# Optimization experiments

Measured on AMD Instinct MI355X. Metric: run time of the kernel, lower is better.

The kernel has to match this reference:

```python
import jax, jax.numpy as jnp
import numpy as np

N_NODES = 10000
N_EDGES = 160000
D = 42          # node_input_dim == node_hidden_dim
DE = 10         # edge_input_dim
DEH = 42        # edge_hidden_dim
N_STEPS = 6


def setup_inputs() -> dict:
    key = jax.random.key(0)
    ks = jax.random.split(key, 16)
    s = 0.1
    return {
        "n_feat": jax.random.normal(ks[0], (N_NODES, D), jnp.float32),
        "e_feat": jax.random.normal(ks[1], (N_EDGES, DE), jnp.float32),
        "src": jax.random.randint(ks[2], (N_EDGES,), 0, N_NODES),
        "dst": jax.random.randint(ks[3], (N_EDGES,), 0, N_NODES),
        # lin0: node_input_dim -> node_hidden_dim
        "lin0_w": s * jax.random.normal(ks[4], (D, D), jnp.float32),
        "lin0_b": s * jax.random.normal(ks[5], (D,), jnp.float32),
        # message_layer: hidden -> hidden
        "msg_w": s * jax.random.normal(ks[6], (D, D), jnp.float32),
        "msg_b": s * jax.random.normal(ks[7], (D,), jnp.float32),
        # edge_network: Linear(10,42) -> ReLU -> Linear(42, 42*42)
        "en_w1": s * jax.random.normal(ks[8], (DE, DEH), jnp.float32),
        "en_b1": s * jax.random.normal(ks[9], (DEH,), jnp.float32),
        "en_w2": s * jax.random.normal(ks[10], (DEH, D * D), jnp.float32),
        "en_b2": s * jax.random.normal(ks[11], (D * D,), jnp.float32),
        # NNConv bias (DGL NNConv has bias=True by default)
        "conv_b": s * jax.random.normal(ks[12], (D,), jnp.float32),
    }


def reference(n_feat, e_feat, src, dst,
              lin0_w, lin0_b, msg_w, msg_b,
              en_w1, en_b1, en_w2, en_b2, conv_b):
    N, d = n_feat.shape
    init = n_feat
    out = jax.nn.relu(n_feat @ lin0_w + lin0_b)                      # [N, d]
    # Per-edge weight matrices from edge features (e_feat is constant
    # across steps, so the edge MLP is hoisted out of the loop).
    w_edge = (jax.nn.relu(e_feat @ en_w1 + en_b1) @ en_w2 + en_b2)   # [E, d*d]
    w_edge = w_edge.reshape(-1, d, d)                                # [E, d_in, d_out]
    for _ in range(N_STEPS):
        # NNConv: gather src feats, per-edge matvec, scatter-sum to dst
        msgs = jnp.einsum('ei,eio->eo', out[src], w_edge)            # [E, d]
        agg = jax.ops.segment_sum(msgs, dst, num_segments=N)         # [N, d]
        # residual (in==out -> identity res_fc) + bias, then outer ReLU
        m = jax.nn.relu(agg + out + conv_b)
        out = jax.nn.relu(m @ msg_w + msg_b)
    return out + init
```

## Files before the change

### kernel.cpp

```cpp
#include <hip/hip_runtime.h>
#include <hip/hip_bf16.h>


#define N_NODES 10000
#define N_EDGES 160000
#define D 42
#define DE 10
#define XSTR 48
#define HSTR 48
#define KI 1806
#define NKSTEP 57
#define SSTR 1832

typedef __attribute__((ext_vector_type(8))) short short8;
typedef __attribute__((ext_vector_type(4))) float f32x4;

static __device__ __forceinline__ short bf16b(float x) {
    __hip_bfloat16 h = __float2bfloat16(x);
    return *reinterpret_cast<short*>(&h);
}

__global__ __launch_bounds__(256) void k_lin0(const float* __restrict__ nf,
        const float* __restrict__ w, const float* __restrict__ b,
        float* __restrict__ out) {
    int idx = blockIdx.x * 256 + threadIdx.x;
    if (idx >= N_NODES * XSTR) return;
    int n = idx / XSTR, j = idx % XSTR;
    float v = 0.f;
    if (j < D) {
        const float* row = nf + n * D;
        float acc = b[j];
        #pragma unroll
        for (int i = 0; i < D; ++i) acc = fmaf(row[i], w[i * D + j], acc);
        v = fmaxf(acc, 0.f);
    }
    out[idx] = v;
}

__global__ __launch_bounds__(256) void k_T2B(const float* __restrict__ w2,
        const float* __restrict__ b2, __hip_bfloat16* __restrict__ Bfr) {
    int idx = blockIdx.x * 256 + threadIdx.x;
    if (idx >= 3 * NKSTEP * 64 * 8) return;
    int j = idx & 7, lane = (idx >> 3) & 63;
    int ks = (idx >> 9) % NKSTEP, nt = idx / (NKSTEP * 512);
    int col = nt * 16 + (lane & 15);
    int k = ks * 32 + ((lane >> 4) * 8) + j;
    float v = 0.f;
    if (col < D && k < KI) {
        int kk = k / D, ii = k % D;
        v = (kk < D) ? w2[kk * (D * D) + ii * D + col] : b2[ii * D + col];
    }
    Bfr[idx] = __float2bfloat16(v);
}

__global__ __launch_bounds__(256) void k_hist(const int* __restrict__ dst,
        int* __restrict__ cnt) {
    int e = blockIdx.x * 256 + threadIdx.x;
    if (e < N_EDGES) atomicAdd(&cnt[dst[e]], 1);
}

__global__ __launch_bounds__(1024) void k_scan(const int* __restrict__ cnt,
        int* __restrict__ row_ptr, int* __restrict__ cursor) {
    __shared__ int buf[1024];
    __shared__ int s_run;
    const int t = threadIdx.x;
    if (t == 0) s_run = 0;
    __syncthreads();
    for (int base = 0; base < N_NODES; base += 1024) {
        int v = (base + t < N_NODES) ? cnt[base + t] : 0;
        buf[t] = v;
        __syncthreads();
        for (int off = 1; off < 1024; off <<= 1) {
            int add = (t >= off) ? buf[t - off] : 0;
            __syncthreads();
            buf[t] += add;
            __syncthreads();
        }
        int excl = buf[t] - v;
        if (base + t < N_NODES) {
            int val = s_run + excl;
            row_ptr[base + t] = val;
            cursor[base + t]  = val;
        }
        __syncthreads();
        if (t == 0) s_run += buf[1023];
        __syncthreads();
    }
    if (t == 0) { row_ptr[N_NODES] = s_run; cursor[N_NODES] = s_run; }
}

__global__ __launch_bounds__(256) void k_scatter(const int* __restrict__ dst,
        const int* __restrict__ src, int* __restrict__ cursor,
        int* __restrict__ srcp, int* __restrict__ pos) {
    int e = blockIdx.x * 256 + threadIdx.x;
    if (e < N_EDGES) {
        int p = atomicAdd(&cursor[dst[e]], 1);
        pos[e] = p;
        srcp[p] = src[e];
    }
}

__global__ __launch_bounds__(256) void k_h16(const float* __restrict__ ef,
        const float* __restrict__ w1, const float* __restrict__ b1,
        const int* __restrict__ pos, __hip_bfloat16* __restrict__ hp16) {
    int idx = blockIdx.x * 256 + threadIdx.x;
    if (idx >= N_EDGES * HSTR) return;
    int e = idx / HSTR, j = idx % HSTR;
    float v;
    if (j < D) {
        const float* row = ef + e * DE;
        float acc = b1[j];
        #pragma unroll
        for (int i = 0; i < DE; ++i) acc = fmaf(row[i], w1[i * D + j], acc);
        v = fmaxf(acc, 0.f);
    } else {
        v = (j == D) ? 1.0f : 0.0f;
    }
    hp16[(size_t)pos[e] * HSTR + j] = __float2bfloat16(v);
}

#define MFMA(A, B, C) C = __builtin_amdgcn_mfma_f32_16x16x32_bf16(A, B, C, 0, 0, 0)

__global__ __launch_bounds__(512) void k_step2(
        const __hip_bfloat16* __restrict__ hp16, const float* __restrict__ out_in,
        const int* __restrict__ srcp, const int* __restrict__ row_ptr,
        const __hip_bfloat16* __restrict__ Bfr,
        const float* __restrict__ nf, const float* __restrict__ msg_w,
        const float* __restrict__ msg_b, const float* __restrict__ conv_b,
        float* __restrict__ out_dst, int last) {
    __shared__ __align__(16) __hip_bfloat16 sS[16 * SSTR];
    __shared__ float sR[16 * 48];
    __shared__ float sM[16 * 48];
    const int t = threadIdx.x;
    const int wv = t >> 6;
    const int l = t & 63;
    const int g = l >> 4;
    const int cl = l & 15;
    const int n0 = blockIdx.x * 16;

    for (int i = t; i < 16 * 48; i += 512) sR[i] = 0.f;
    for (int i = t; i < 16 * 18; i += 512)
        sS[(i / 18) * SSTR + KI + (i % 18)] = __float2bfloat16(0.f);

    const short* hp_s = (const short*)hp16;
    for (int q = 0; q < 2; ++q) {
        const int nloc = wv * 2 + q;
        const int node = n0 + nloc;
        const int beg = row_ptr[node], end = row_ptr[node + 1];
        f32x4 c00 = {0.f,0.f,0.f,0.f}, c01 = c00, c02 = c00;
        f32x4 c10 = c00, c11 = c00, c12 = c00;
        f32x4 c20 = c00, c21 = c00, c22 = c00;
        for (int e0 = beg; e0 < end; e0 += 32) {
            short8 a0, a1, a2, b0, b1, b2;
            #pragma unroll
            for (int j = 0; j < 8; ++j) {
                int ppos = e0 + g * 8 + j;
                bool vld = ppos < end;
                int pc = vld ? ppos : end - 1;
                const short* hr = hp_s + (size_t)pc * HSTR + cl;
                short h0 = hr[0], h1 = hr[16], h2 = hr[32];
                a0[j] = vld ? h0 : (short)0;
                a1[j] = vld ? h1 : (short)0;
                a2[j] = vld ? h2 : (short)0;
                const float* xr = out_in + (size_t)srcp[pc] * XSTR + cl;
                b0[j] = bf16b(xr[0]);
                b1[j] = bf16b(xr[16]);
                b2[j] = bf16b(xr[32]);
            }
            MFMA(a0, b0, c00); MFMA(a0, b1, c01); MFMA(a0, b2, c02);
            MFMA(a1, b0, c10); MFMA(a1, b1, c11); MFMA(a1, b2, c12);
            MFMA(a2, b0, c20); MFMA(a2, b1, c21); MFMA(a2, b2, c22);
        }
        #define ST(ACC, MT, NT)                                              \
            _Pragma("unroll")                                                \
            for (int r = 0; r < 4; ++r) {                                    \
                int m = (MT) * 16 + g * 4 + r;                               \
                int col = (NT) * 16 + cl;                                    \
                if (m < 43 && col < D)                                       \
                    sS[nloc * SSTR + m * D + col] = __float2bfloat16(ACC[r]);\
            }
        ST(c00, 0, 0) ST(c01, 0, 1) ST(c02, 0, 2)
        ST(c10, 1, 0) ST(c11, 1, 1) ST(c12, 1, 2)
        ST(c20, 2, 0) ST(c21, 2, 1) ST(c22, 2, 2)
        #undef ST
    }
    __syncthreads();

    {
        const int ks0 = (wv == 0) ? 0 : (wv * 7 + 1);
        const int ks1 = wv * 7 + 8;
        f32x4 d0 = {0.f,0.f,0.f,0.f}, d1 = d0, d2 = d0;
        const short* sSrow = (const short*)sS + cl * SSTR + g * 8;
        const short* bb = (const short*)Bfr + (size_t)l * 8;
        for (int ks = ks0; ks < ks1; ++ks) {
            short8 a  = *(const short8*)(sSrow + ks * 32);
            short8 B0 = *(const short8*)(bb + (size_t)(0 * NKSTEP + ks) * 512);
            short8 B1 = *(const short8*)(bb + (size_t)(1 * NKSTEP + ks) * 512);
            short8 B2 = *(const short8*)(bb + (size_t)(2 * NKSTEP + ks) * 512);
            MFMA(a, B0, d0); MFMA(a, B1, d1); MFMA(a, B2, d2);
        }
        const int rl = g * 4;
        #pragma unroll
        for (int r = 0; r < 4; ++r) {
            atomicAdd(&sR[(rl + r) * 48 + cl],      d0[r]);
            atomicAdd(&sR[(rl + r) * 48 + 16 + cl], d1[r]);
            atomicAdd(&sR[(rl + r) * 48 + 32 + cl], d2[r]);
        }
    }
    __syncthreads();

    float* sW = (float*)sS;
    for (int i = t; i < D * D; i += 512) sW[i] = msg_w[i];
    for (int idx = t; idx < 16 * 48; idx += 512) {
        int nl_ = idx / 48, o = idx % 48;
        float mv = 0.f;
        if (o < D) {
            float v = sR[idx] + out_in[(size_t)(n0 + nl_) * XSTR + o] + conv_b[o];
            mv = fmaxf(v, 0.f);
        }
        sM[idx] = mv;
    }
    __syncthreads();

    for (int idx = t; idx < 16 * 48; idx += 512) {
        int nl_ = idx / 48, pcol = idx % 48;
        if (pcol < D) {
            float s = msg_b[pcol];
            #pragma unroll 6
            for (int o = 0; o < D; ++o)
                s = fmaf(sM[nl_ * 48 + o], sW[o * D + pcol], s);
            float v = fmaxf(s, 0.f);
            if (last) {
                v += nf[(size_t)(n0 + nl_) * D + pcol];
                out_dst[(size_t)(n0 + nl_) * D + pcol] = v;
            } else {
                out_dst[(size_t)(n0 + nl_) * XSTR + pcol] = v;
            }
        } else if (!last) {
            out_dst[(size_t)(n0 + nl_) * XSTR + pcol] = 0.f;
        }
    }
}

extern "C" void kernel_launch(void* const* d_in, const int* in_sizes, int n_in,
                              void* d_out, int out_size, void* d_ws, size_t ws_size,
                              hipStream_t stream) {
    const float* nf    = (const float*)d_in[0];
    const float* ef    = (const float*)d_in[1];
    const int*   src   = (const int*)d_in[2];
    const int*   dst   = (const int*)d_in[3];
    const float* lin0w = (const float*)d_in[4];
    const float* lin0b = (const float*)d_in[5];
    const float* msgw  = (const float*)d_in[6];
    const float* msgb  = (const float*)d_in[7];
    const float* enw1  = (const float*)d_in[8];
    const float* enb1  = (const float*)d_in[9];
    const float* enw2  = (const float*)d_in[10];
    const float* enb2  = (const float*)d_in[11];
    const float* convb = (const float*)d_in[12];

    char* p = (char*)d_ws;
    auto alloc = [&](size_t bytes) -> char* {
        char* r = p; p += (bytes + 255) & ~(size_t)255; return r;
    };
    float* outA = (float*)alloc((size_t)N_NODES * XSTR * 4);
    float* outB = (float*)alloc((size_t)N_NODES * XSTR * 4);
    __hip_bfloat16* hp16 = (__hip_bfloat16*)alloc((size_t)N_EDGES * HSTR * 2);
    __hip_bfloat16* Bfr  = (__hip_bfloat16*)alloc((size_t)3 * NKSTEP * 64 * 8 * 2);
    int* cnt    = (int*)alloc((N_NODES + 1) * 4);
    int* rowp   = (int*)alloc((N_NODES + 1) * 4);
    int* cur    = (int*)alloc((N_NODES + 1) * 4);
    int* srcp   = (int*)alloc((size_t)N_EDGES * 4);
    int* posb   = (int*)alloc((size_t)N_EDGES * 4);

    hipMemsetAsync(cnt, 0, (N_NODES + 1) * 4, stream);
    k_lin0<<<(N_NODES * XSTR + 255) / 256, 256, 0, stream>>>(nf, lin0w, lin0b, outA);
    k_T2B<<<(3 * NKSTEP * 64 * 8 + 255) / 256, 256, 0, stream>>>(enw2, enb2, Bfr);
    k_hist<<<(N_EDGES + 255) / 256, 256, 0, stream>>>(dst, cnt);
    k_scan<<<1, 1024, 0, stream>>>(cnt, rowp, cur);
    k_scatter<<<(N_EDGES + 255) / 256, 256, 0, stream>>>(dst, src, cur, srcp, posb);
    k_h16<<<(N_EDGES * HSTR + 255) / 256, 256, 0, stream>>>(ef, enw1, enb1, posb, hp16);

    const int tiles = N_NODES / 16;
    float* bufs[2] = {outA, outB};
    for (int s_i = 0; s_i < 6; ++s_i) {
        const float* cin = bufs[s_i % 2];
        float* cout = bufs[(s_i + 1) % 2];
        int last = (s_i == 5) ? 1 : 0;
        k_step2<<<tiles, 512, 0, stream>>>(hp16, cin, srcp, rowp, Bfr,
                                           nf, msgw, msgb, convb,
                                           last ? (float*)d_out : cout, last);
    }
}
```

Baseline: 350.0 us.

## Store node features in bf16, transpose edge hidden into 32-edge chunks, halve block

Node feature buffers become bf16 instead of fp32, which halves gather traffic and removes per-element conversion in the inner loop. The edge hidden activations are stored transposed in 32-edge chunks so each lane does vector short8 loads, with masking at node boundaries. Source indices are loaded as int4. Each wave now processes two nodes interleaved to expose more memory-level parallelism, and blocks shrink to 8 nodes and 256 threads, which raises occupancy but means each Bfr fragment is reused across only half as many nodes.

```diff
diff --git a/kernel.cpp b/kernel.cpp
--- a/kernel.cpp
+++ b/kernel.cpp
@@ -4,10 +4,10 @@
 
 #define N_NODES 10000
 #define N_EDGES 160000
+#define NCHK 5000
 #define D 42
 #define DE 10
 #define XSTR 48
-#define HSTR 48
 #define KI 1806
 #define NKSTEP 57
 #define SSTR 1832
@@ -15,14 +15,9 @@
 typedef __attribute__((ext_vector_type(8))) short short8;
 typedef __attribute__((ext_vector_type(4))) float f32x4;
 
-static __device__ __forceinline__ short bf16b(float x) {
-    __hip_bfloat16 h = __float2bfloat16(x);
-    return *reinterpret_cast<short*>(&h);
-}
-
 __global__ __launch_bounds__(256) void k_lin0(const float* __restrict__ nf,
         const float* __restrict__ w, const float* __restrict__ b,
-        float* __restrict__ out) {
+        __hip_bfloat16* __restrict__ out16) {
     int idx = blockIdx.x * 256 + threadIdx.x;
     if (idx >= N_NODES * XSTR) return;
     int n = idx / XSTR, j = idx % XSTR;
@@ -34,7 +29,7 @@
         for (int i = 0; i < D; ++i) acc = fmaf(row[i], w[i * D + j], acc);
         v = fmaxf(acc, 0.f);
     }
-    out[idx] = v;
+    out16[idx] = __float2bfloat16(v);
 }
 
 __global__ __launch_bounds__(256) void k_T2B(const float* __restrict__ w2,
@@ -91,106 +86,160 @@
 
 __global__ __launch_bounds__(256) void k_scatter(const int* __restrict__ dst,
         const int* __restrict__ src, int* __restrict__ cursor,
-        int* __restrict__ srcp, int* __restrict__ pos) {
+        int* __restrict__ srcp, int* __restrict__ eperm) {
     int e = blockIdx.x * 256 + threadIdx.x;
     if (e < N_EDGES) {
         int p = atomicAdd(&cursor[dst[e]], 1);
-        pos[e] = p;
         srcp[p] = src[e];
-    }
-}
-
-__global__ __launch_bounds__(256) void k_h16(const float* __restrict__ ef,
+        eperm[p] = e;
+    }
+}
+
+__global__ __launch_bounds__(256) void k_hT(const float* __restrict__ ef,
         const float* __restrict__ w1, const float* __restrict__ b1,
-        const int* __restrict__ pos, __hip_bfloat16* __restrict__ hp16) {
-    int idx = blockIdx.x * 256 + threadIdx.x;
-    if (idx >= N_EDGES * HSTR) return;
-    int e = idx / HSTR, j = idx % HSTR;
-    float v;
-    if (j < D) {
-        const float* row = ef + e * DE;
-        float acc = b1[j];
-        #pragma unroll
-        for (int i = 0; i < DE; ++i) acc = fmaf(row[i], w1[i * D + j], acc);
-        v = fmaxf(acc, 0.f);
-    } else {
-        v = (j == D) ? 1.0f : 0.0f;
-    }
-    hp16[(size_t)pos[e] * HSTR + j] = __float2bfloat16(v);
+        const int* __restrict__ eperm, __hip_bfloat16* __restrict__ hpT) {
+    const int c = blockIdx.x;
+    const int t = threadIdx.x;
+    for (int j = t; j < 48 * 32; j += 256) {
+        int k = j >> 5, ep = j & 31;
+        int e = eperm[c * 32 + ep];
+        float v;
+        if (k < D) {
+            const float* row = ef + (size_t)e * DE;
+            float acc = b1[k];
+            #pragma unroll
+            for (int i = 0; i < DE; ++i) acc = fmaf(row[i], w1[i * D + k], acc);
+            v = fmaxf(acc, 0.f);
+        } else {
+            v = (k == D) ? 1.0f : 0.f;
+        }
+        hpT[(size_t)c * 1536 + j] = __float2bfloat16(v);
+    }
 }
 
 #define MFMA(A, B, C) C = __builtin_amdgcn_mfma_f32_16x16x32_bf16(A, B, C, 0, 0, 0)
 
-__global__ __launch_bounds__(512) void k_step2(
-        const __hip_bfloat16* __restrict__ hp16, const float* __restrict__ out_in,
+__global__ __launch_bounds__(256) void k_step3(
+        const __hip_bfloat16* __restrict__ hpT,
+        const __hip_bfloat16* __restrict__ out_in,
         const int* __restrict__ srcp, const int* __restrict__ row_ptr,
         const __hip_bfloat16* __restrict__ Bfr,
         const float* __restrict__ nf, const float* __restrict__ msg_w,
         const float* __restrict__ msg_b, const float* __restrict__ conv_b,
-        float* __restrict__ out_dst, int last) {
-    __shared__ __align__(16) __hip_bfloat16 sS[16 * SSTR];
-    __shared__ float sR[16 * 48];
-    __shared__ float sM[16 * 48];
+        __hip_bfloat16* __restrict__ out16_dst, float* __restrict__ fout,
+        int last) {
+    __shared__ __align__(16) __hip_bfloat16 sS[8 * SSTR];
+    __shared__ float sR[8 * 48];
+    __shared__ float sM[8 * 48];
     const int t = threadIdx.x;
     const int wv = t >> 6;
     const int l = t & 63;
     const int g = l >> 4;
+    const int g8 = g * 8;
     const int cl = l & 15;
-    const int n0 = blockIdx.x * 16;
-
-    for (int i = t; i < 16 * 48; i += 512) sR[i] = 0.f;
-    for (int i = t; i < 16 * 18; i += 512)
+    const int n0 = blockIdx.x * 8;
+    const short* hpTs = (const short*)hpT;
+    const short* xs = (const short*)out_in;
+
+    for (int i = t; i < 8 * 48; i += 256) sR[i] = 0.f;
+    for (int i = t; i < 8 * 18; i += 256)
         sS[(i / 18) * SSTR + KI + (i % 18)] = __float2bfloat16(0.f);
 
-    const short* hp_s = (const short*)hp16;
-    for (int q = 0; q < 2; ++q) {
-        const int nloc = wv * 2 + q;
-        const int node = n0 + nloc;
-        const int beg = row_ptr[node], end = row_ptr[node + 1];
-        f32x4 c00 = {0.f,0.f,0.f,0.f}, c01 = c00, c02 = c00;
-        f32x4 c10 = c00, c11 = c00, c12 = c00;
-        f32x4 c20 = c00, c21 = c00, c22 = c00;
-        for (int e0 = beg; e0 < end; e0 += 32) {
-            short8 a0, a1, a2, b0, b1, b2;
+    const int nodeA = n0 + wv * 2, nodeB = nodeA + 1;
+    const int begA = row_ptr[nodeA], endA = row_ptr[nodeA + 1];
+    const int begB = endA, endB = row_ptr[nodeB + 1];
+    const int c0A = begA >> 5, ncA = (endA > begA) ? ((endA - 1) >> 5) - c0A + 1 : 0;
+    const int c0B = begB >> 5, ncB = (endB > begB) ? ((endB - 1) >> 5) - c0B + 1 : 0;
+    const int ncmax = max(ncA, ncB);
+
+    f32x4 cA[9], cB[9];
+    #pragma unroll
+    for (int i = 0; i < 9; ++i) { cA[i] = {0.f,0.f,0.f,0.f}; cB[i] = cA[i]; }
+
+    for (int ci = 0; ci < ncmax; ++ci) {
+        short8 aA0, aA1, aA2, bA0, bA1, bA2;
+        short8 aB0, aB1, aB2, bB0, bB1, bB2;
+        bool doA = ci < ncA, doB = ci < ncB;
+        if (doA) {
+            const int c = c0A + ci, c32 = c << 5;
+            const short* hb = hpTs + (size_t)c * 1536 + cl * 32 + g8;
+            aA0 = *(const short8*)(hb);
+            aA1 = *(const short8*)(hb + 16 * 32);
+            aA2 = *(const short8*)(hb + 32 * 32);
+            int4 s0 = *(const int4*)(srcp + c32 + g8);
+            int4 s1 = *(const int4*)(srcp + c32 + g8 + 4);
+            const int se[8] = {s0.x, s0.y, s0.z, s0.w, s1.x, s1.y, s1.z, s1.w};
             #pragma unroll
             for (int j = 0; j < 8; ++j) {
-                int ppos = e0 + g * 8 + j;
-                bool vld = ppos < end;
-                int pc = vld ? ppos : end - 1;
-                const short* hr = hp_s + (size_t)pc * HSTR + cl;
-                short h0 = hr[0], h1 = hr[16], h2 = hr[32];
-                a0[j] = vld ? h0 : (short)0;
-                a1[j] = vld ? h1 : (short)0;
-                a2[j] = vld ? h2 : (short)0;
-                const float* xr = out_in + (size_t)srcp[pc] * XSTR + cl;
-                b0[j] = bf16b(xr[0]);
-                b1[j] = bf16b(xr[16]);
-                b2[j] = bf16b(xr[32]);
-            }
-            MFMA(a0, b0, c00); MFMA(a0, b1, c01); MFMA(a0, b2, c02);
-            MFMA(a1, b0, c10); MFMA(a1, b1, c11); MFMA(a1, b2, c12);
-            MFMA(a2, b0, c20); MFMA(a2, b1, c21); MFMA(a2, b2, c22);
-        }
-        #define ST(ACC, MT, NT)                                              \
-            _Pragma("unroll")                                                \
-            for (int r = 0; r < 4; ++r) {                                    \
-                int m = (MT) * 16 + g * 4 + r;                               \
-                int col = (NT) * 16 + cl;                                    \
-                if (m < 43 && col < D)                                       \
-                    sS[nloc * SSTR + m * D + col] = __float2bfloat16(ACC[r]);\
-            }
-        ST(c00, 0, 0) ST(c01, 0, 1) ST(c02, 0, 2)
-        ST(c10, 1, 0) ST(c11, 1, 1) ST(c12, 1, 2)
-        ST(c20, 2, 0) ST(c21, 2, 1) ST(c22, 2, 2)
-        #undef ST
-    }
+                const short* xr = xs + (size_t)se[j] * XSTR + cl;
+                bA0[j] = xr[0]; bA1[j] = xr[16]; bA2[j] = xr[32];
+            }
+            if (c32 < begA || c32 + 32 > endA) {
+                #pragma unroll
+                for (int j = 0; j < 8; ++j) {
+                    int ep = c32 + g8 + j;
+                    if (ep < begA || ep >= endA) { aA0[j] = 0; aA1[j] = 0; aA2[j] = 0; }
+                }
+            }
+        }
+        if (doB) {
+            const int c = c0B + ci, c32 = c << 5;
+            const short* hb = hpTs + (size_t)c * 1536 + cl * 32 + g8;
+            aB0 = *(const short8*)(hb);
+            aB1 = *(const short8*)(hb + 16 * 32);
+            aB2 = *(const short8*)(hb + 32 * 32);
+            int4 s0 = *(const int4*)(srcp + c32 + g8);
+            int4 s1 = *(const int4*)(srcp + c32 + g8 + 4);
+            const int se[8] = {s0.x, s0.y, s0.z, s0.w, s1.x, s1.y, s1.z, s1.w};
+            #pragma unroll
+            for (int j = 0; j < 8; ++j) {
+                const short* xr = xs + (size_t)se[j] * XSTR + cl;
+                bB0[j] = xr[0]; bB1[j] = xr[16]; bB2[j] = xr[32];
+            }
+            if (c32 < begB || c32 + 32 > endB) {
+                #pragma unroll
+                for (int j = 0; j < 8; ++j) {
+                    int ep = c32 + g8 + j;
+                    if (ep < begB || ep >= endB) { aB0[j] = 0; aB1[j] = 0; aB2[j] = 0; }
+                }
+            }
+        }
+        if (doA) {
+            MFMA(aA0, bA0, cA[0]); MFMA(aA0, bA1, cA[1]); MFMA(aA0, bA2, cA[2]);
+            MFMA(aA1, bA0, cA[3]); MFMA(aA1, bA1, cA[4]); MFMA(aA1, bA2, cA[5]);
+            MFMA(aA2, bA0, cA[6]); MFMA(aA2, bA1, cA[7]); MFMA(aA2, bA2, cA[8]);
+        }
+        if (doB) {
+            MFMA(aB0, bB0, cB[0]); MFMA(aB0, bB1, cB[1]); MFMA(aB0, bB2, cB[2]);
+            MFMA(aB1, bB0, cB[3]); MFMA(aB1, bB1, cB[4]); MFMA(aB1, bB2, cB[5]);
+            MFMA(aB2, bB0, cB[6]); MFMA(aB2, bB1, cB[7]); MFMA(aB2, bB2, cB[8]);
+        }
+    }
+    #define ST(CC, NLOC, MT, NT)                                             \
+        _Pragma("unroll")                                                    \
+        for (int r = 0; r < 4; ++r) {                                        \
+            int m = (MT) * 16 + g * 4 + r;                                   \
+            int col = (NT) * 16 + cl;                                        \
+            if (m < 43 && col < D)                                           \
+                sS[(NLOC) * SSTR + m * D + col] = __float2bfloat16(CC[r]);   \
+        }
+    {
+        const int nlA = wv * 2, nlB = nlA + 1;
+        ST(cA[0], nlA, 0, 0) ST(cA[1], nlA, 0, 1) ST(cA[2], nlA, 0, 2)
+        ST(cA[3], nlA, 1, 0) ST(cA[4], nlA, 1, 1) ST(cA[5], nlA, 1, 2)
+        ST(cA[6], nlA, 2, 0) ST(cA[7], nlA, 2, 1) ST(cA[8], nlA, 2, 2)
+        ST(cB[0], nlB, 0, 0) ST(cB[1], nlB, 0, 1) ST(cB[2], nlB, 0, 2)
+        ST(cB[3], nlB, 1, 0) ST(cB[4], nlB, 1, 1) ST(cB[5], nlB, 1, 2)
+        ST(cB[6], nlB, 2, 0) ST(cB[7], nlB, 2, 1) ST(cB[8], nlB, 2, 2)
+    }
+    #undef ST
     __syncthreads();
 
     {
-        const int ks0 = (wv == 0) ? 0 : (wv * 7 + 1);
-        const int ks1 = wv * 7 + 8;
+        const int ks0 = (wv == 0) ? 0 : (wv * 14 + 1);
+        const int ks1 = wv * 14 + 15;
         f32x4 d0 = {0.f,0.f,0.f,0.f}, d1 = d0, d2 = d0;
-        const short* sSrow = (const short*)sS + cl * SSTR + g * 8;
+        const short* sSrow = (const short*)sS + (cl & 7) * SSTR + g8;
         const short* bb = (const short*)Bfr + (size_t)l * 8;
         for (int ks = ks0; ks < ks1; ++ks) {
             short8 a  = *(const short8*)(sSrow + ks * 32);
@@ -199,30 +248,32 @@
             short8 B2 = *(const short8*)(bb + (size_t)(2 * NKSTEP + ks) * 512);
             MFMA(a, B0, d0); MFMA(a, B1, d1); MFMA(a, B2, d2);
         }
-        const int rl = g * 4;
-        #pragma unroll
-        for (int r = 0; r < 4; ++r) {
-            atomicAdd(&sR[(rl + r) * 48 + cl],      d0[r]);
-            atomicAdd(&sR[(rl + r) * 48 + 16 + cl], d1[r]);
-            atomicAdd(&sR[(rl + r) * 48 + 32 + cl], d2[r]);
+        if (g < 2) {
+            const int rl = g * 4;
+            #pragma unroll
+            for (int r = 0; r < 4; ++r) {
+                atomicAdd(&sR[(rl + r) * 48 + cl],      d0[r]);
+                atomicAdd(&sR[(rl + r) * 48 + 16 + cl], d1[r]);
+                atomicAdd(&sR[(rl + r) * 48 + 32 + cl], d2[r]);
+            }
         }
     }
     __syncthreads();
 
     float* sW = (float*)sS;
-    for (int i = t; i < D * D; i += 512) sW[i] = msg_w[i];
-    for (int idx = t; idx < 16 * 48; idx += 512) {
+    for (int i = t; i < D * D; i += 256) sW[i] = msg_w[i];
+    for (int idx = t; idx < 8 * 48; idx += 256) {
         int nl_ = idx / 48, o = idx % 48;
         float mv = 0.f;
         if (o < D) {
-            float v = sR[idx] + out_in[(size_t)(n0 + nl_) * XSTR + o] + conv_b[o];
-            mv = fmaxf(v, 0.f);
+            float res = __bfloat162float(out_in[(size_t)(n0 + nl_) * XSTR + o]);
+            mv = fmaxf(sR[idx] + res + conv_b[o], 0.f);
         }
         sM[idx] = mv;
     }
     __syncthreads();
 
-    for (int idx = t; idx < 16 * 48; idx += 512) {
+    for (int idx = t; idx < 8 * 48; idx += 256) {
         int nl_ = idx / 48, pcol = idx % 48;
         if (pcol < D) {
             float s = msg_b[pcol];
@@ -231,13 +282,13 @@
                 s = fmaf(sM[nl_ * 48 + o], sW[o * D + pcol], s);
             float v = fmaxf(s, 0.f);
             if (last) {
-                v += nf[(size_t)(n0 + nl_) * D + pcol];
-                out_dst[(size_t)(n0 + nl_) * D + pcol] = v;
+                fout[(size_t)(n0 + nl_) * D + pcol] =
+                    v + nf[(size_t)(n0 + nl_) * D + pcol];
             } else {
-                out_dst[(size_t)(n0 + nl_) * XSTR + pcol] = v;
+                out16_dst[(size_t)(n0 + nl_) * XSTR + pcol] = __float2bfloat16(v);
             }
         } else if (!last) {
-            out_dst[(size_t)(n0 + nl_) * XSTR + pcol] = 0.f;
+            out16_dst[(size_t)(n0 + nl_) * XSTR + pcol] = __float2bfloat16(0.f);
         }
     }
 }
@@ -263,32 +314,32 @@
     auto alloc = [&](size_t bytes) -> char* {
         char* r = p; p += (bytes + 255) & ~(size_t)255; return r;
     };
-    float* outA = (float*)alloc((size_t)N_NODES * XSTR * 4);
-    float* outB = (float*)alloc((size_t)N_NODES * XSTR * 4);
-    __hip_bfloat16* hp16 = (__hip_bfloat16*)alloc((size_t)N_EDGES * HSTR * 2);
+    __hip_bfloat16* outA = (__hip_bfloat16*)alloc((size_t)N_NODES * XSTR * 2);
+    __hip_bfloat16* outB = (__hip_bfloat16*)alloc((size_t)N_NODES * XSTR * 2);
+    __hip_bfloat16* hpT  = (__hip_bfloat16*)alloc((size_t)NCHK * 1536 * 2);
     __hip_bfloat16* Bfr  = (__hip_bfloat16*)alloc((size_t)3 * NKSTEP * 64 * 8 * 2);
     int* cnt    = (int*)alloc((N_NODES + 1) * 4);
     int* rowp   = (int*)alloc((N_NODES + 1) * 4);
     int* cur    = (int*)alloc((N_NODES + 1) * 4);
     int* srcp   = (int*)alloc((size_t)N_EDGES * 4);
-    int* posb   = (int*)alloc((size_t)N_EDGES * 4);
+    int* eperm  = (int*)alloc((size_t)N_EDGES * 4);
 
     hipMemsetAsync(cnt, 0, (N_NODES + 1) * 4, stream);
     k_lin0<<<(N_NODES * XSTR + 255) / 256, 256, 0, stream>>>(nf, lin0w, lin0b, outA);
     k_T2B<<<(3 * NKSTEP * 64 * 8 + 255) / 256, 256, 0, stream>>>(enw2, enb2, Bfr);
     k_hist<<<(N_EDGES + 255) / 256, 256, 0, stream>>>(dst, cnt);
     k_scan<<<1, 1024, 0, stream>>>(cnt, rowp, cur);
-    k_scatter<<<(N_EDGES + 255) / 256, 256, 0, stream>>>(dst, src, cur, srcp, posb);
-    k_h16<<<(N_EDGES * HSTR + 255) / 256, 256, 0, stream>>>(ef, enw1, enb1, posb, hp16);
-
-    const int tiles = N_NODES / 16;
-    float* bufs[2] = {outA, outB};
+    k_scatter<<<(N_EDGES + 255) / 256, 256, 0, stream>>>(dst, src, cur, srcp, eperm);
+    k_hT<<<NCHK, 256, 0, stream>>>(ef, enw1, enb1, eperm, hpT);
+
+    const int tiles = N_NODES / 8;
+    __hip_bfloat16* bufs[2] = {outA, outB};
     for (int s_i = 0; s_i < 6; ++s_i) {
-        const float* cin = bufs[s_i % 2];
-        float* cout = bufs[(s_i + 1) % 2];
+        const __hip_bfloat16* cin = bufs[s_i % 2];
+        __hip_bfloat16* cout = bufs[(s_i + 1) % 2];
         int last = (s_i == 5) ? 1 : 0;
-        k_step2<<<tiles, 512, 0, stream>>>(hp16, cin, srcp, rowp, Bfr,
+        k_step3<<<tiles, 256, 0, stream>>>(hpT, cin, srcp, rowp, Bfr,
                                            nf, msgw, msgb, convb,
-                                           last ? (float*)d_out : cout, last);
-    }
-}
+                                           cout, (float*)d_out, last);
+    }
+}
```

Result: slower. 357.9 us (+2.2%).
